# Kernel optimization log

Hardware: AMD Instinct MI355X
Metric: run time of the kernel (lower is better)

## Reference

```python
import jax, jax.numpy as jnp
import numpy as np

NUM_EMB = 100000
EMB_DIM = 128
NUM_FIELD = 23
SEQ = 3
BATCH = 16384
FEAT = NUM_FIELD * EMB_DIM  # 2944
N_EXPERT = 8
EXPERT_SIZE = 1024
TOWER_SIZE = 512
N_GATE = 3  # counterfact_mode == 'DR'
EPS = 1e-15


def setup_inputs() -> dict:
    key = jax.random.key(0)
    ks = jax.random.split(key, 10)
    inputs = jax.random.randint(ks[0], (NUM_FIELD, BATCH, SEQ), 0, NUM_EMB, dtype=jnp.int32)
    emb_table = jax.random.normal(ks[1], (NUM_EMB, EMB_DIM), dtype=jnp.float32) * 0.02
    emb_table = emb_table.at[0].set(0.0)  # padding_idx=0
    expert_w = jax.random.normal(ks[2], (N_EXPERT, FEAT, EXPERT_SIZE), dtype=jnp.float32) * (FEAT ** -0.5)
    expert_b = jnp.zeros((N_EXPERT, EXPERT_SIZE), dtype=jnp.float32)
    gate_w = jax.random.normal(ks[3], (N_GATE, FEAT, N_EXPERT), dtype=jnp.float32) * (FEAT ** -0.5)
    gate_b = jnp.zeros((N_GATE, N_EXPERT), dtype=jnp.float32)
    tower_w = jax.random.normal(ks[4], (N_GATE, EXPERT_SIZE, TOWER_SIZE), dtype=jnp.float32) * (EXPERT_SIZE ** -0.5)
    tower_b = jnp.zeros((N_GATE, TOWER_SIZE), dtype=jnp.float32)
    out_w = jax.random.normal(ks[5], (N_GATE, TOWER_SIZE, 2), dtype=jnp.float32) * (TOWER_SIZE ** -0.5)
    out_b = jnp.zeros((N_GATE, 2), dtype=jnp.float32)
    return {"inputs": inputs, "emb_table": emb_table,
            "expert_w": expert_w, "expert_b": expert_b,
            "gate_w": gate_w, "gate_b": gate_b,
            "tower_w": tower_w, "tower_b": tower_b,
            "out_w": out_w, "out_b": out_b}


def reference(inputs, emb_table, expert_w, expert_b, gate_w, gate_b, tower_w, tower_b, out_w, out_b):
    F_, B, L = inputs.shape
    # embedding lookup + sum-pool per field: [F,B,L,D] -> [F,B,D]
    pooled = jnp.take(emb_table, inputs, axis=0).sum(axis=2)
    # concat fields along feature dim: [B, F*D]
    concat = jnp.transpose(pooled, (1, 0, 2)).reshape(B, F_ * emb_table.shape[1])
    # experts: [B, E, H]
    expert_out = jax.nn.relu(jnp.einsum('bf,efh->beh', concat, expert_w) + expert_b[None])
    # gates: softmax over experts, [B, G, E]
    gates = jax.nn.softmax(jnp.einsum('bf,gfe->bge', concat, gate_w) + gate_b[None], axis=-1)
    # gated expert mixture: [B, G, H]
    mixed = jnp.einsum('bge,beh->bgh', gates, expert_out)
    # towers: [B, G, T]
    tower = jax.nn.relu(jnp.einsum('bgh,ght->bgt', mixed, tower_w) + tower_b[None])
    # tower outs: softmax + clamp, [B, G, 2]
    outs = jax.nn.softmax(jnp.einsum('bgt,gto->bgo', tower, out_w) + out_b[None], axis=-1)
    outs = jnp.clip(outs, EPS, 1.0 - EPS)
    ctr_out = outs[:, 0]
    cvr_out = outs[:, 1]
    ctr_prop_one = ctr_out[:, 1:2]
    cvr_prop_one = cvr_out[:, 1:2]
    ctcvr_prop_one = ctr_prop_one * cvr_prop_one
    ctcvr_prop = jnp.concatenate([1.0 - ctcvr_prop_one, ctcvr_prop_one], axis=1)
    imp_prop_one = outs[:, 2][:, 1:2]
    return (ctr_out, ctr_prop_one, cvr_out, cvr_prop_one, ctcvr_prop, ctcvr_prop_one, imp_prop_one)
```

## Files before the change

### kernel.cpp

```cpp
#include <hip/hip_runtime.h>
#include <hip/hip_bf16.h>
#include <stdint.h>

#define NUM_B   16384
#define FIELDS  23
#define EMBD    128
#define FEATD   2944
#define NEXP    8
#define ESIZE   1024
#define TSIZE   512
#define NGATE   3

using short8 = __attribute__((ext_vector_type(8))) short;
using f32x4  = __attribute__((ext_vector_type(4))) float;

__device__ __forceinline__ unsigned short f2bf(float x) {
  union { float f; unsigned u; } c; c.f = x;
  unsigned r = (c.u + 0x7fffu + ((c.u >> 16) & 1u)) >> 16;
  return (unsigned short)r;
}
__device__ __forceinline__ float bf2f(unsigned short x) {
  union { unsigned u; float f; } c; c.u = ((unsigned)x) << 16;
  return c.f;
}

__device__ __forceinline__ void g2l16(const void* g, void* l) {
  __builtin_amdgcn_global_load_lds(
      (const __attribute__((address_space(1))) void*)g,
      (__attribute__((address_space(3))) void*)l,
      16, 0, 0);
}

#define BAR()   __builtin_amdgcn_s_barrier()
#define LGKM0() asm volatile("s_waitcnt lgkmcnt(0)" ::: "memory")

__global__ __launch_bounds__(256) void k_transpose(const float* __restrict__ src,
                                                   unsigned short* __restrict__ dst,
                                                   int R, int C) {
  long zoff = (long)blockIdx.z * R * C;
  src += zoff; dst += zoff;
  __shared__ float t[32][33];
  int tx = threadIdx.x, ty = threadIdx.y;
  int r0 = blockIdx.y * 32, c0 = blockIdx.x * 32;
#pragma unroll
  for (int i = 0; i < 4; ++i) {
    int r = r0 + ty + i * 8;
    t[ty + i * 8][tx] = src[(long)r * C + c0 + tx];
  }
  __syncthreads();
#pragma unroll
  for (int i = 0; i < 4; ++i) {
    int c = c0 + ty + i * 8;
    dst[(long)c * R + r0 + tx] = f2bf(t[tx][ty + i * 8]);
  }
}

__global__ __launch_bounds__(256) void k1_pool(const int* __restrict__ idx,
                                               const float* __restrict__ emb,
                                               unsigned short* __restrict__ concat,
                                               int b0) {
  int tid = threadIdx.x;
  int p = tid >> 5, l = tid & 31;
  int f = blockIdx.y;
  int bl = blockIdx.x * 8 + p;
  int b = b0 + bl;
  const int* ip = idx + ((long)f * NUM_B + b) * 3;
  long i0 = ip[0], i1 = ip[1], i2 = ip[2];
  float4 a = *((const float4*)(emb + i0 * EMBD) + l);
  float4 c = *((const float4*)(emb + i1 * EMBD) + l);
  float4 d = *((const float4*)(emb + i2 * EMBD) + l);
  float sx = a.x + c.x + d.x, sy = a.y + c.y + d.y;
  float sz = a.z + c.z + d.z, sw = a.w + c.w + d.w;
  ushort4 o;
  o.x = f2bf(sx); o.y = f2bf(sy); o.z = f2bf(sz); o.w = f2bf(sw);
  *(ushort4*)(concat + (long)bl * FEATD + f * EMBD + l * 4) = o;
}

__global__ __launch_bounds__(256) void k2_gates(const unsigned short* __restrict__ concat,
                                                const float* __restrict__ gw,
                                                const float* __restrict__ gb,
                                                float* __restrict__ gates) {
  __shared__ float part[4][64][24];
  int tid = threadIdx.x;
  int r = tid & 63;
  int q = __builtin_amdgcn_readfirstlane(tid >> 6);
  int bl = blockIdx.x * 64 + r;
  float acc[24];
#pragma unroll
  for (int i = 0; i < 24; ++i) acc[i] = 0.f;
  const int kpt = FEATD / 4;
  int k0 = q * kpt;
  const unsigned short* arow = concat + (long)bl * FEATD;
  for (int kk = k0; kk < k0 + kpt; kk += 8) {
    short8 a8 = *(const short8*)(arow + kk);
    const float* w0 = gw + (long)kk * 8;
#pragma unroll
    for (int jj = 0; jj < 8; ++jj) {
      float av = bf2f((unsigned short)a8[jj]);
      const float* wp = w0 + jj * 8;
#pragma unroll
      for (int e = 0; e < 8; ++e) {
        acc[e]      += av * wp[e];
        acc[8 + e]  += av * wp[FEATD * 8 + e];
        acc[16 + e] += av * wp[2 * FEATD * 8 + e];
      }
    }
  }
#pragma unroll
  for (int i = 0; i < 24; ++i) part[q][r][i] = acc[i];
  __syncthreads();
  if (tid < 64) {
    float tot[24];
#pragma unroll
    for (int i = 0; i < 24; ++i)
      tot[i] = part[0][tid][i] + part[1][tid][i] + part[2][tid][i] + part[3][tid][i] + gb[i];
    float* gout = gates + (long)(blockIdx.x * 64 + tid) * 24;
#pragma unroll
    for (int g = 0; g < 3; ++g) {
      float m = tot[g * 8];
#pragma unroll
      for (int e = 1; e < 8; ++e) m = fmaxf(m, tot[g * 8 + e]);
      float ex[8]; float s = 0.f;
#pragma unroll
      for (int e = 0; e < 8; ++e) { ex[e] = expf(tot[g * 8 + e] - m); s += ex[e]; }
      float inv = 1.f / s;
#pragma unroll
      for (int e = 0; e < 8; ++e) gout[g * 8 + e] = ex[e] * inv;
    }
  }
}

#define RD_A(buf, m, Pk) (*(const short8*)((buf) + aRow + (m) * 1024 + (Pk)))
#define RD_B(buf, n, Pk) (*(const short8*)((buf) + bRow + (n) * 1024 + (Pk)))

#define PHASE(AB, BB, m0v, m1v, LOADB, ...)                                    \
  {                                                                            \
    if (LOADB) {                                                               \
      _Pragma("unroll") for (int n = 0; n < 4; ++n) {                          \
        Bf[n][0] = RD_B(BB, n, Pk0);                                           \
        Bf[n][1] = RD_B(BB, n, Pk1);                                           \
      }                                                                        \
    }                                                                          \
    short8 A00 = RD_A(AB, m0v, Pk0), A01 = RD_A(AB, m0v, Pk1);                 \
    short8 A10 = RD_A(AB, m1v, Pk0), A11 = RD_A(AB, m1v, Pk1);                 \
    __VA_ARGS__;                                                               \
    BAR(); LGKM0();                                                            \
    __builtin_amdgcn_s_setprio(1);                                             \
    _Pragma("unroll") for (int n = 0; n < 4; ++n) {                            \
      acc[m0v][n] = __builtin_amdgcn_mfma_f32_16x16x32_bf16(A00, Bf[n][0], acc[m0v][n], 0, 0, 0); \
      acc[m0v][n] = __builtin_amdgcn_mfma_f32_16x16x32_bf16(A01, Bf[n][1], acc[m0v][n], 0, 0, 0); \
      acc[m1v][n] = __builtin_amdgcn_mfma_f32_16x16x32_bf16(A10, Bf[n][0], acc[m1v][n], 0, 0, 0); \
      acc[m1v][n] = __builtin_amdgcn_mfma_f32_16x16x32_bf16(A11, Bf[n][1], acc[m1v][n], 0, 0, 0); \
    }                                                                          \
    __builtin_amdgcn_s_setprio(0);                                             \
  }

__global__ __launch_bounds__(512, 2) void gemm8(
    const unsigned short* __restrict__ A, long sA,
    const unsigned short* __restrict__ Bt, long sB,
    const float* __restrict__ bias, long sBias,
    unsigned short* __restrict__ C, long sC,
    int K, int ldc) {
  __shared__ unsigned short lds[65536];

  const int z = blockIdx.z;
  A += (long)z * sA; Bt += (long)z * sB; bias += (long)z * sBias; C += (long)z * sC;

  const int tid = threadIdx.x;
  const int wid = tid >> 6, lane = tid & 63;
  const int wm = wid >> 2, wn = wid & 3;
  const int bm = blockIdx.x << 8, bn = blockIdx.y << 8;

  unsigned short* a0 = lds;
  unsigned short* a1 = lds + 16384;
  unsigned short* b0 = lds + 32768;
  unsigned short* b1 = lds + 49152;

  const int srcK = (((lane & 7) * 16) ^ ((lane >> 3) << 4)) >> 1;
  const int lsub = lane >> 3;
  const int ldst = lane * 8;

  const int aRow = (wm * 128 + (lane & 15)) * 64;
  const int bRow = (wn * 64 + (lane & 15)) * 64;
  const int Pk0 = ((((lane >> 4) << 4)) ^ ((lane & 7) << 4)) >> 1;
  const int Pk1 = ((64 + ((lane >> 4) << 4)) ^ ((lane & 7) << 4)) >> 1;

  auto stA = [&](unsigned short* dbuf, int tk, int q) {
    int rb = (wid < 4) ? (q * 32 + wid * 8) : (128 + q * 32 + (wid - 4) * 8);
    g2l16(A + (long)(bm + rb + lsub) * K + tk * 64 + srcK, dbuf + rb * 64 + ldst);
  };
  auto stB = [&](unsigned short* dbuf, int tk, int q) {
    int rb = q * 64 + wid * 8;
    g2l16(Bt + (long)(bn + rb + lsub) * K + tk * 64 + srcK, dbuf + rb * 64 + ldst);
  };

  f32x4 acc[8][4];
#pragma unroll
  for (int i = 0; i < 8; ++i)
#pragma unroll
    for (int j = 0; j < 4; ++j) acc[i][j] = (f32x4){0.f, 0.f, 0.f, 0.f};

  stA(a0, 0, 0); stA(a0, 0, 1); stA(a0, 0, 2); stA(a0, 0, 3);
  stB(b0, 0, 0); stB(b0, 0, 1); stB(b0, 0, 2); stB(b0, 0, 3);
  stA(a1, 1, 0); stA(a1, 1, 1); stA(a1, 1, 2);
  asm volatile("s_waitcnt vmcnt(0)" ::: "memory");
  BAR();

  const int NITER = K >> 7;
  for (int i = 0; i < NITER; ++i) {
    const int t1 = 2 * i + 1, t2 = 2 * i + 2, t3 = 2 * i + 3;
    const bool more = (i + 1 < NITER);
    short8 Bf[4][2];
    PHASE(a0, b0, 0, 1, 1, stA(a1, t1, 3); stB(b1, t1, 0); stB(b1, t1, 1));
    BAR();
    PHASE(a0, b0, 2, 3, 0, stB(b1, t1, 2); stB(b1, t1, 3));
    BAR();
    PHASE(a0, b0, 4, 5, 0, if (more) { stA(a0, t2, 0); stA(a0, t2, 1); });
    BAR();
    PHASE(a0, b0, 6, 7, 0, if (more) stA(a0, t2, 2));
    if (more) asm volatile("s_waitcnt vmcnt(3)" ::: "memory");
    else      asm volatile("s_waitcnt vmcnt(0)" ::: "memory");
    BAR();
    PHASE(a1, b1, 0, 1, 1, if (more) { stA(a0, t2, 3); stB(b0, t2, 0); });
    BAR();
    PHASE(a1, b1, 2, 3, 0, if (more) { stB(b0, t2, 1); stB(b0, t2, 2); });
    BAR();
    PHASE(a1, b1, 4, 5, 0, if (more) { stB(b0, t2, 3); stA(a1, t3, 0); });
    BAR();
    PHASE(a1, b1, 6, 7, 0, if (more) { stA(a1, t3, 1); stA(a1, t3, 2); });
    if (more) asm volatile("s_waitcnt vmcnt(3)" ::: "memory");
    BAR();
  }

#pragma unroll
  for (int m = 0; m < 8; ++m) {
    long row0 = bm + wm * 128 + m * 16 + (lane >> 4) * 4;
#pragma unroll
    for (int n = 0; n < 4; ++n) {
      long col = bn + wn * 64 + n * 16 + (lane & 15);
      float bv = bias[col];
#pragma unroll
      for (int r = 0; r < 4; ++r) {
        float v = acc[m][n][r] + bv;
        v = fmaxf(v, 0.f);
        C[(row0 + r) * ldc + col] = f2bf(v);
      }
    }
  }
}

__global__ __launch_bounds__(256) void k4_mix(const unsigned short* __restrict__ eo,
                                              const float* __restrict__ gates,
                                              unsigned short* __restrict__ mixed,
                                              int Bc) {
  int tid = threadIdx.x;
  int bl = blockIdx.x * 2 + (tid >> 7);
  int h8 = (tid & 127) * 8;
  const float* gp = gates + (long)bl * 24;
  float o0[8], o1[8], o2[8];
#pragma unroll
  for (int x = 0; x < 8; ++x) { o0[x] = 0.f; o1[x] = 0.f; o2[x] = 0.f; }
  const unsigned short* ep = eo + (long)bl * (NEXP * ESIZE) + h8;
#pragma unroll
  for (int e = 0; e < 8; ++e) {
    short8 v = *(const short8*)(ep + e * ESIZE);
    float g0 = gp[e], g1 = gp[8 + e], g2 = gp[16 + e];
#pragma unroll
    for (int x = 0; x < 8; ++x) {
      float fv = bf2f((unsigned short)v[x]);
      o0[x] += g0 * fv; o1[x] += g1 * fv; o2[x] += g2 * fv;
    }
  }
  long base = (long)bl * ESIZE + h8;
  short8 w0, w1, w2;
#pragma unroll
  for (int x = 0; x < 8; ++x) {
    w0[x] = (short)f2bf(o0[x]); w1[x] = (short)f2bf(o1[x]); w2[x] = (short)f2bf(o2[x]);
  }
  *(short8*)(mixed + base) = w0;
  *(short8*)(mixed + (long)Bc * ESIZE + base) = w1;
  *(short8*)(mixed + 2L * Bc * ESIZE + base) = w2;
}

__global__ __launch_bounds__(256) void k6_out(const unsigned short* __restrict__ tower,
                                              const float* __restrict__ ow,
                                              const float* __restrict__ ob,
                                              float* __restrict__ out,
                                              int b0, int Bc) {
  int tid = threadIdx.x;
  int wid = tid >> 6, lane = tid & 63;
  int bl = blockIdx.x * 4 + wid;
  long b = (long)b0 + bl;
  float l0[3], l1[3];
#pragma unroll
  for (int g = 0; g < 3; ++g) {
    short8 t8 = *(const short8*)(tower + ((long)g * Bc + bl) * TSIZE + lane * 8);
    const float2* wp = (const float2*)(ow + g * (TSIZE * 2)) + lane * 8;
    float s0 = 0.f, s1 = 0.f;
#pragma unroll
    for (int x = 0; x < 8; ++x) {
      float a = bf2f((unsigned short)t8[x]);
      float2 w = wp[x];
      s0 += a * w.x; s1 += a * w.y;
    }
#pragma unroll
    for (int off = 32; off > 0; off >>= 1) {
      s0 += __shfl_xor(s0, off);
      s1 += __shfl_xor(s1, off);
    }
    l0[g] = s0 + ob[g * 2];
    l1[g] = s1 + ob[g * 2 + 1];
  }
  if (lane == 0) {
    float p0[3], p1[3];
#pragma unroll
    for (int g = 0; g < 3; ++g) {
      float d = l1[g] - l0[g];
      float e1 = 1.f / (1.f + expf(-d));
      float e0 = 1.f / (1.f + expf(d));
      p0[g] = fminf(fmaxf(e0, 1e-15f), 1.f - 1e-15f);
      p1[g] = fminf(fmaxf(e1, 1e-15f), 1.f - 1e-15f);
    }
    float ct = p1[0] * p1[1];
    out[b * 2]              = p0[0];
    out[b * 2 + 1]          = p1[0];
    out[32768 + b]          = p1[0];
    out[49152 + b * 2]      = p0[1];
    out[49152 + b * 2 + 1]  = p1[1];
    out[81920 + b]          = p1[1];
    out[98304 + b * 2]      = 1.f - ct;
    out[98304 + b * 2 + 1]  = ct;
    out[131072 + b]         = ct;
    out[147456 + b]         = p1[2];
  }
}

extern "C" void kernel_launch(void* const* d_in, const int* in_sizes, int n_in,
                              void* d_out, int out_size, void* d_ws, size_t ws_size,
                              hipStream_t stream) {
  (void)in_sizes; (void)n_in; (void)out_size;
  const int*   idx      = (const int*)d_in[0];
  const float* emb      = (const float*)d_in[1];
  const float* expert_w = (const float*)d_in[2];
  const float* expert_b = (const float*)d_in[3];
  const float* gate_w   = (const float*)d_in[4];
  const float* gate_b   = (const float*)d_in[5];
  const float* tower_w  = (const float*)d_in[6];
  const float* tower_b  = (const float*)d_in[7];
  const float* out_w    = (const float*)d_in[8];
  const float* out_b    = (const float*)d_in[9];
  float* out = (float*)d_out;

  const size_t P_EOW  = (size_t)NEXP * ESIZE * FEATD * 2;
  const size_t P_TWT  = (size_t)NGATE * TSIZE * ESIZE * 2;
  const size_t P      = P_EOW + P_TWT;
  const size_t PER_B  = 31584;
  int NC = 1;
  while (NC < 64 && P + (size_t)(NUM_B / NC) * PER_B > ws_size) NC <<= 1;
  if (P + (size_t)(NUM_B / NC) * PER_B > ws_size) return;
  const int Bc = NUM_B / NC;

  char* ws = (char*)d_ws;
  unsigned short* eoW     = (unsigned short*)(ws);
  unsigned short* towerWt = (unsigned short*)(ws + P_EOW);
  size_t off = P;
  unsigned short* concat  = (unsigned short*)(ws + off); off += (size_t)Bc * 5888;
  float*          gates   = (float*)(ws + off);          off += (size_t)Bc * 96;
  unsigned short* eo      = (unsigned short*)(ws + off); off += (size_t)Bc * 16384;
  unsigned short* mixed   = (unsigned short*)(ws + off); off += (size_t)Bc * 6144;
  unsigned short* tower   = (unsigned short*)(ws + off);

  k_transpose<<<dim3(ESIZE / 32, FEATD / 32, NEXP), dim3(32, 8), 0, stream>>>(
      expert_w, eoW, FEATD, ESIZE);
  k_transpose<<<dim3(TSIZE / 32, ESIZE / 32, NGATE), dim3(32, 8), 0, stream>>>(
      tower_w, towerWt, ESIZE, TSIZE);

  for (int c = 0; c < NC; ++c) {
    const int b0 = c * Bc;
    k1_pool<<<dim3(Bc / 8, FIELDS), 256, 0, stream>>>(idx, emb, concat, b0);
    k2_gates<<<dim3(Bc / 64), 256, 0, stream>>>(concat, gate_w, gate_b, gates);
    gemm8<<<dim3(Bc / 256, ESIZE / 256, NEXP), 512, 0, stream>>>(
        concat, 0L, eoW, (long)ESIZE * FEATD, expert_b, (long)ESIZE,
        eo, (long)ESIZE, FEATD, NEXP * ESIZE);
    k4_mix<<<dim3(Bc / 2), 256, 0, stream>>>(eo, gates, mixed, Bc);
    gemm8<<<dim3(Bc / 256, TSIZE / 256, NGATE), 512, 0, stream>>>(
        mixed, (long)Bc * ESIZE, towerWt, (long)TSIZE * ESIZE, tower_b, (long)TSIZE,
        tower, (long)Bc * TSIZE, ESIZE, TSIZE);
    k6_out<<<dim3(Bc / 4), 256, 0, stream>>>(tower, out_w, out_b, out, b0, Bc);
  }
}
```

Before: 1.312 ms.

## Remap GEMM workgroups per XCD and issue B tile loads one stage earlier

Workgroup IDs are remapped so that consecutive logical tiles land on the same XCD, which is meant to improve L2 reuse of A/B tiles across the chiplets. The load schedule is also reordered: B tiles for the next k-step are issued earlier (a prologue prefetch of b1, and b0 loads moved up into the phases), and the wait counts are relaxed from vmcnt(3) to vmcnt(7). This keeps more global loads in flight so memory latency is hidden better. The cost is tighter correctness reasoning about which LDS buffers are still being read when the early B writes land.

Result: slower. 1.373 ms (+4.6%).

```diff
diff --git a/kernel.cpp b/kernel.cpp
--- a/kernel.cpp
+++ b/kernel.cpp
@@ -155,6 +155,9 @@
     __builtin_amdgcn_s_setprio(0);                                             \
   }
 
+#define VMC7() asm volatile("s_waitcnt vmcnt(7)" ::: "memory")
+#define VMC0() asm volatile("s_waitcnt vmcnt(0)" ::: "memory")
+
 __global__ __launch_bounds__(512, 2) void gemm8(
     const unsigned short* __restrict__ A, long sA,
     const unsigned short* __restrict__ Bt, long sB,
@@ -163,13 +166,22 @@
     int K, int ldc) {
   __shared__ unsigned short lds[65536];
 
-  const int z = blockIdx.z;
+  const int nwg = gridDim.x * gridDim.y * gridDim.z;
+  const int id = blockIdx.x + gridDim.x * (blockIdx.y + gridDim.y * blockIdx.z);
+  const int qq = nwg >> 3, rr = nwg & 7;
+  const int xcd = id & 7, pos = id >> 3;
+  const int w = (xcd < rr ? xcd * (qq + 1) : rr * (qq + 1) + (xcd - rr) * qq) + pos;
+  const int bx = w % gridDim.x;
+  const int tmpw = w / gridDim.x;
+  const int by = tmpw % gridDim.y;
+  const int z = tmpw / gridDim.y;
+
   A += (long)z * sA; Bt += (long)z * sB; bias += (long)z * sBias; C += (long)z * sC;
 
   const int tid = threadIdx.x;
   const int wid = tid >> 6, lane = tid & 63;
   const int wm = wid >> 2, wn = wid & 3;
-  const int bm = blockIdx.x << 8, bn = blockIdx.y << 8;
+  const int bm = bx << 8, bn = by << 8;
 
   unsigned short* a0 = lds;
   unsigned short* a1 = lds + 16384;
@@ -202,8 +214,9 @@
 
   stA(a0, 0, 0); stA(a0, 0, 1); stA(a0, 0, 2); stA(a0, 0, 3);
   stB(b0, 0, 0); stB(b0, 0, 1); stB(b0, 0, 2); stB(b0, 0, 3);
+  stB(b1, 1, 0); stB(b1, 1, 1); stB(b1, 1, 2); stB(b1, 1, 3);
   stA(a1, 1, 0); stA(a1, 1, 1); stA(a1, 1, 2);
-  asm volatile("s_waitcnt vmcnt(0)" ::: "memory");
+  VMC7();
   BAR();
 
   const int NITER = K >> 7;
@@ -211,24 +224,24 @@
     const int t1 = 2 * i + 1, t2 = 2 * i + 2, t3 = 2 * i + 3;
     const bool more = (i + 1 < NITER);
     short8 Bf[4][2];
-    PHASE(a0, b0, 0, 1, 1, stA(a1, t1, 3); stB(b1, t1, 0); stB(b1, t1, 1));
-    BAR();
-    PHASE(a0, b0, 2, 3, 0, stB(b1, t1, 2); stB(b1, t1, 3));
-    BAR();
-    PHASE(a0, b0, 4, 5, 0, if (more) { stA(a0, t2, 0); stA(a0, t2, 1); });
+    PHASE(a0, b0, 0, 1, 1, stA(a1, t1, 3));
+    BAR();
+    PHASE(a0, b0, 2, 3, 0, if (more) { stB(b0, t2, 0); stB(b0, t2, 1); });
+    BAR();
+    PHASE(a0, b0, 4, 5, 0,
+          if (more) { stB(b0, t2, 2); stB(b0, t2, 3); stA(a0, t2, 0); stA(a0, t2, 1); });
     BAR();
     PHASE(a0, b0, 6, 7, 0, if (more) stA(a0, t2, 2));
-    if (more) asm volatile("s_waitcnt vmcnt(3)" ::: "memory");
-    else      asm volatile("s_waitcnt vmcnt(0)" ::: "memory");
-    BAR();
-    PHASE(a1, b1, 0, 1, 1, if (more) { stA(a0, t2, 3); stB(b0, t2, 0); });
-    BAR();
-    PHASE(a1, b1, 2, 3, 0, if (more) { stB(b0, t2, 1); stB(b0, t2, 2); });
-    BAR();
-    PHASE(a1, b1, 4, 5, 0, if (more) { stB(b0, t2, 3); stA(a1, t3, 0); });
+    if (more) VMC7(); else VMC0();
+    BAR();
+    PHASE(a1, b1, 0, 1, 1, if (more) stA(a0, t2, 3));
+    BAR();
+    PHASE(a1, b1, 2, 3, 0, if (more) { stB(b1, t3, 0); stB(b1, t3, 1); });
+    BAR();
+    PHASE(a1, b1, 4, 5, 0, if (more) { stB(b1, t3, 2); stB(b1, t3, 3); stA(a1, t3, 0); });
     BAR();
     PHASE(a1, b1, 6, 7, 0, if (more) { stA(a1, t3, 1); stA(a1, t3, 2); });
-    if (more) asm volatile("s_waitcnt vmcnt(3)" ::: "memory");
+    if (more) VMC7();
     BAR();
   }
 
```
